# Performance work log

Measured on AMD Instinct MI355X. Metric: run time of the kernel, lower is better.

The kernel has to match this reference:

```python
import jax, jax.numpy as jnp
import numpy as np

B, S, E, H, VP, L, T = 256, 256, 1024, 1024, 8, 64, 16


def setup_inputs() -> dict:
    key = jax.random.key(0)
    ks = jax.random.split(key, 10)
    image = jax.random.normal(ks[0], (B, S, E), jnp.float32)
    view_position = jax.random.uniform(ks[1], (B, VP), jnp.float32)
    label = (jax.random.uniform(ks[2], (B, T + 1, L)) > 0.5).astype(jnp.float32)
    # lengths sorted descending (length_sorted_rnn decorator), max forced to T+1
    length = jnp.sort(jax.random.randint(ks[3], (B,), 2, T + 2))[::-1]
    length = length.at[0].set(T + 1)
    def lin(k, out_d, in_d):
        return jax.random.normal(k, (out_d, in_d), jnp.float32) * (1.0 / np.sqrt(in_d)).astype(np.float32)
    IN = E + VP + 1 + L  # 1097: lstm_sizes = [embedding, view_position, 1, label]
    FC_OUT = L + H + 1 + 1  # 1090: fc_sizes = [label, hidden, 1, 1]
    return {
        'image': image, 'view_position': view_position, 'label': label, 'length': length,
        'W_h': lin(ks[4], H, E), 'b_h': jnp.zeros((H,), jnp.float32),
        'W_m': lin(ks[5], H, E), 'b_m': jnp.zeros((H,), jnp.float32),
        'W_ih': lin(ks[6], 4 * H, IN), 'W_hh': lin(ks[7], 4 * H, H),
        'b_ih': jnp.zeros((4 * H,), jnp.float32), 'b_hh': jnp.zeros((4 * H,), jnp.float32),
        'W_fc': lin(ks[8], FC_OUT, H), 'b_fc': jnp.zeros((FC_OUT,), jnp.float32),
    }


def reference(image, view_position, label, length, W_h, b_h, W_m, b_m,
              W_ih, W_hh, b_ih, b_hh, W_fc, b_fc):
    # Dropout is identity (inference). image: (B,S,E)
    image_mean = image.mean(axis=1)                      # (B,E)
    h0 = jnp.tanh(image_mean @ W_h.T + b_h)              # (B,H)
    m0 = jnp.tanh(image_mean @ W_m.T + b_m)              # (B,H)
    n_steps = label.shape[1] - 1
    bsz = image_mean.shape[0]

    def step(carry, inp):
        h, m = carry
        lab_t, t = inp
        begin = jnp.where(t == 0, 1.0, 0.0) * jnp.ones((bsz, 1), image_mean.dtype)
        x = jnp.concatenate([image_mean, view_position, begin, lab_t], axis=1)  # (B, 1097)
        gates = x @ W_ih.T + b_ih + h @ W_hh.T + b_hh    # (B, 4H)
        i, f, g, o = jnp.split(gates, 4, axis=1)
        m2 = jax.nn.sigmoid(f) * m + jax.nn.sigmoid(i) * jnp.tanh(g)
        h2 = jax.nn.sigmoid(o) * jnp.tanh(m2)
        out = h2 @ W_fc.T + b_fc                         # (B, L+H+2)
        topic = jax.nn.relu(out[:, L:L + H])
        stop = jax.nn.sigmoid(out[:, L + H:L + H + 1])
        temp = jnp.exp(out[:, L + H + 1:])
        return (h2, m2), jnp.concatenate([topic, stop, temp], axis=1)

    labels_tm = jnp.swapaxes(label[:, :n_steps], 0, 1)   # (T,B,L) time-major
    _, outs = jax.lax.scan(step, (h0, m0), (labels_tm, jnp.arange(n_steps)))
    # pad_sequence semantics: entries with t >= length-1 are zero padding
    mask = (jnp.arange(n_steps)[:, None] < (length - 1)[None, :]).astype(outs.dtype)
    return outs * mask[:, :, None]                       # (T, B, H+2) = [topic|stop|temp]
```

## Files before the change

kernel.cpp:

```cpp
#include <hip/hip_runtime.h>
#include <stdint.h>

typedef unsigned short u16;
typedef __attribute__((ext_vector_type(8))) short v8s;
typedef __attribute__((ext_vector_type(4))) float v4f;

__device__ __forceinline__ u16 f2bf(float f) {
  uint32_t x = __float_as_uint(f);
  return (u16)((x + 0x7fffu + ((x >> 16) & 1u)) >> 16);
}
__device__ __forceinline__ float bf2f(u16 u) {
  return __uint_as_float(((uint32_t)u) << 16);
}
__device__ __forceinline__ float sigf(float x) { return 1.f / (1.f + __expf(-x)); }

__device__ __forceinline__ v4f mfma16(v8s a, v8s b, v4f c) {
  return __builtin_amdgcn_mfma_f32_16x16x32_bf16(a, b, c, 0, 0, 0);
}

__device__ __forceinline__ void gll16(const u16* src, u16* ldsdst) {
  __builtin_amdgcn_global_load_lds(
      reinterpret_cast<__attribute__((address_space(1))) uint32_t*>(
          reinterpret_cast<uintptr_t>(src)),
      reinterpret_cast<__attribute__((address_space(3))) uint32_t*>(
          reinterpret_cast<uintptr_t>(ldsdst)),
      16, 0, 0);
}

__device__ __forceinline__ size_t fpoff(int row, int k, int KT) {
  return ((size_t)(((row >> 4) * KT + (k >> 6)) * 2 + ((k >> 5) & 1)) * 64 +
          ((k >> 3) & 3) * 16 + (row & 15)) * 8 + (k & 7);
}

__device__ __forceinline__ void load8(const float* p, float* f) {
  float4 a = *(const float4*)p;
  float4 b = *(const float4*)(p + 4);
  f[0]=a.x; f[1]=a.y; f[2]=a.z; f[3]=a.w; f[4]=b.x; f[5]=b.y; f[6]=b.z; f[7]=b.w;
}
__device__ __forceinline__ void store8bf(u16* dst, const float* f) {
  u16 t[8];
#pragma unroll
  for (int i = 0; i < 8; ++i) t[i] = f2bf(f[i]);
  *(v8s*)dst = *(const v8s*)t;
}

__global__ __launch_bounds__(256) void k_zero(unsigned* __restrict__ ctr) {
  ctr[blockIdx.x * 256 + threadIdx.x] = 0u;
}

__global__ __launch_bounds__(256) void k_convert(
    const float* __restrict__ Wh, const float* __restrict__ Wm,
    const float* __restrict__ Wih, const float* __restrict__ Whh,
    const float* __restrict__ Wfc, const float* __restrict__ label,
    u16* __restrict__ wcomb, u16* __restrict__ whhb, u16* __restrict__ wfcb,
    u16* __restrict__ wlabb, u16* __restrict__ labb) {
  int64_t u = (int64_t)blockIdx.x * 256 + threadIdx.x;
  float f[8];
  if (u < 786432) {
    int lu = (int)u;
    int r15 = lu & 15, q = (lu >> 4) & 3, s = (lu >> 6) & 1, tile = lu >> 7;
    int tk = tile & 15, tr = tile >> 4;
    int row = tr * 16 + r15, k = tk * 64 + s * 32 + q * 8;
    if (row < 1024) load8(Wh + (size_t)row * 1024 + k, f);
    else if (row < 2048) load8(Wm + (size_t)(row - 1024) * 1024 + k, f);
    else {
      const float* p = Wih + (size_t)(row - 2048) * 1097 + k;
#pragma unroll
      for (int i = 0; i < 8; ++i) f[i] = p[i];
    }
    store8bf(wcomb + (size_t)lu * 8, f);
  } else if (u < 1310720) {
    int lu = (int)(u - 786432);
    int r15 = lu & 15, q = (lu >> 4) & 3, s = (lu >> 6) & 1, tile = lu >> 7;
    int tk = tile & 15, tr = tile >> 4;
    int row = tr * 16 + r15, k = tk * 64 + s * 32 + q * 8;
    load8(Whh + (size_t)row * 1024 + k, f);
    store8bf(whhb + (size_t)lu * 8, f);
  } else if (u < 1458176) {
    int lu = (int)(u - 1310720);
    int r15 = lu & 15, q = (lu >> 4) & 3, s = (lu >> 6) & 1, tile = lu >> 7;
    int tk = tile & 15, tr = tile >> 4;
    int row = tr * 16 + r15, k = tk * 64 + s * 32 + q * 8;
    if (row < 1090) load8(Wfc + (size_t)row * 1024 + k, f);
    else {
#pragma unroll
      for (int i = 0; i < 8; ++i) f[i] = 0.f;
    }
    store8bf(wfcb + (size_t)lu * 8, f);
  } else if (u < 1490944) {
    int lu = (int)(u - 1458176);
    int r15 = lu & 15, q = (lu >> 4) & 3, s = (lu >> 6) & 1, tile = lu >> 7;
    int row = tile * 16 + r15, k = s * 32 + q * 8;
    const float* p = Wih + (size_t)row * 1097 + 1033 + k;
#pragma unroll
    for (int i = 0; i < 8; ++i) f[i] = p[i];
    store8bf(wlabb + (size_t)lu * 8, f);
  } else {
    int lu = (int)(u - 1490944);
    int r15 = lu & 15, q = (lu >> 4) & 3, s = (lu >> 6) & 1, tile = lu >> 7;
    int row = tile * 16 + r15, k = s * 32 + q * 8;
    int t = row >> 8, b = row & 255;
    load8(label + ((size_t)b * 17 + t) * 64 + k, f);
    store8bf(labb + (size_t)lu * 8, f);
  }
}

__global__ __launch_bounds__(256) void k_mean1(const float* __restrict__ image,
                                               float4* __restrict__ pacc) {
  int bi = blockIdx.x;
  int b = bi >> 3, oct = bi & 7, tid = threadIdx.x;
  const float4* src = (const float4*)image + (size_t)b * 65536 + (size_t)oct * 32 * 256 + tid;
  float4 s = make_float4(0.f, 0.f, 0.f, 0.f);
#pragma unroll 8
  for (int ss = 0; ss < 32; ++ss) {
    float4 v = src[(size_t)ss * 256];
    s.x += v.x; s.y += v.y; s.z += v.z; s.w += v.w;
  }
  pacc[(size_t)bi * 256 + tid] = s;
}
__global__ __launch_bounds__(256) void k_mean2(const float4* __restrict__ pacc,
                                               u16* __restrict__ meanbf) {
  int b = blockIdx.x, tid = threadIdx.x;
  float4 s = make_float4(0.f, 0.f, 0.f, 0.f);
#pragma unroll
  for (int q = 0; q < 8; ++q) {
    float4 v = pacc[((size_t)b * 8 + q) * 256 + tid];
    s.x += v.x; s.y += v.y; s.z += v.z; s.w += v.w;
  }
  const float inv = 1.f / 256.f;
  int k = tid * 4;
  ushort4 o;
  o.x = f2bf(s.x * inv); o.y = f2bf(s.y * inv);
  o.z = f2bf(s.z * inv); o.w = f2bf(s.w * inv);
  *(ushort4*)&meanbf[fpoff(b, k, 16)] = o;
}

__global__ __launch_bounds__(256) void k_gemm_init(
    const u16* __restrict__ meanbf, const u16* __restrict__ wcomb,
    const float* __restrict__ bh, const float* __restrict__ bm,
    const float* __restrict__ bih, const float* __restrict__ bhh,
    const float* __restrict__ vp, const float* __restrict__ Wih,
    u16* __restrict__ hbuf, float* __restrict__ mbuf, float* __restrict__ basebuf) {
  __shared__ alignas(16) u16 lA[4 * 1024];
  __shared__ alignas(16) u16 lB[4 * 1024];
  const int tid = threadIdx.x, lane = tid & 63, wid = tid >> 6;
  const int bm0 = (blockIdx.x & 3) * 64;
  const int bn0 = (blockIdx.x >> 2) * 64;
  const int wr = wid >> 1, wc = wid & 1;
  v4f acc[2][2];
#pragma unroll
  for (int i = 0; i < 2; ++i)
#pragma unroll
    for (int j = 0; j < 2; ++j) acc[i][j] = (v4f){0.f, 0.f, 0.f, 0.f};

  for (int kt = 0; kt < 16; ++kt) {
    const u16* asrc = meanbf + ((size_t)((bm0 >> 4) + wid) * 16 + kt) * 1024 + lane * 8;
    gll16(asrc, lA + wid * 1024);
    gll16(asrc + 512, lA + wid * 1024 + 512);
    const u16* bsrc = wcomb + ((size_t)((bn0 >> 4) + wid) * 16 + kt) * 1024 + lane * 8;
    gll16(bsrc, lB + wid * 1024);
    gll16(bsrc + 512, lB + wid * 1024 + 512);
    __syncthreads();
#pragma unroll
    for (int s = 0; s < 2; ++s) {
      v8s a0 = *(const v8s*)&lA[(size_t)(wr * 2) * 1024 + s * 512 + lane * 8];
      v8s a1 = *(const v8s*)&lA[(size_t)(wr * 2 + 1) * 1024 + s * 512 + lane * 8];
      v8s b0 = *(const v8s*)&lB[(size_t)(wc * 2) * 1024 + s * 512 + lane * 8];
      v8s b1 = *(const v8s*)&lB[(size_t)(wc * 2 + 1) * 1024 + s * 512 + lane * 8];
      acc[0][0] = mfma16(a0, b0, acc[0][0]);
      acc[0][1] = mfma16(a0, b1, acc[0][1]);
      acc[1][0] = mfma16(a1, b0, acc[1][0]);
      acc[1][1] = mfma16(a1, b1, acc[1][1]);
    }
    __syncthreads();
  }
#pragma unroll
  for (int fm = 0; fm < 2; ++fm)
#pragma unroll
    for (int fn = 0; fn < 2; ++fn)
#pragma unroll
      for (int rg = 0; rg < 4; ++rg) {
        int row = bm0 + wr * 32 + fm * 16 + ((lane >> 4) << 2) + rg;
        int col = bn0 + wc * 32 + fn * 16 + (lane & 15);
        float v = acc[fm][fn][rg];
        if (col < 1024) {
          hbuf[fpoff(row, col, 16)] = f2bf(tanhf(v + bh[col]));
        } else if (col < 2048) {
          int nn = col - 1024;
          mbuf[(size_t)row * 1024 + nn] = tanhf(v + bm[nn]);
        } else {
          int j = col - 2048;
          float sv = v + bih[j] + bhh[j];
#pragma unroll
          for (int q = 0; q < 8; ++q)
            sv += vp[row * 8 + q] * Wih[(size_t)j * 1097 + 1024 + q];
          basebuf[(size_t)row * 4096 + j] = sv;
        }
      }
}

__global__ __launch_bounds__(256) void k_basefull(
    const u16* __restrict__ labb, const u16* __restrict__ wlabb,
    const float* __restrict__ basebuf, const float* __restrict__ Wih,
    u16* __restrict__ bfull) {
  __shared__ alignas(16) u16 lA[4 * 1024];
  __shared__ alignas(16) u16 lB[4 * 1024];
  const int tid = threadIdx.x, lane = tid & 63, wid = tid >> 6;
  const int bm0 = (blockIdx.x & 63) * 64;
  const int bn0 = (blockIdx.x >> 6) * 64;
  const int wr = wid >> 1, wc = wid & 1;
  v4f acc[2][2];
#pragma unroll
  for (int i = 0; i < 2; ++i)
#pragma unroll
    for (int j = 0; j < 2; ++j) acc[i][j] = (v4f){0.f, 0.f, 0.f, 0.f};

  const u16* asrc = labb + (size_t)((bm0 >> 4) + wid) * 1024 + lane * 8;
  gll16(asrc, lA + wid * 1024);
  gll16(asrc + 512, lA + wid * 1024 + 512);
  const u16* bsrc = wlabb + (size_t)((bn0 >> 4) + wid) * 1024 + lane * 8;
  gll16(bsrc, lB + wid * 1024);
  gll16(bsrc + 512, lB + wid * 1024 + 512);
  __syncthreads();
#pragma unroll
  for (int s = 0; s < 2; ++s) {
    v8s a0 = *(const v8s*)&lA[(size_t)(wr * 2) * 1024 + s * 512 + lane * 8];
    v8s a1 = *(const v8s*)&lA[(size_t)(wr * 2 + 1) * 1024 + s * 512 + lane * 8];
    v8s b0 = *(const v8s*)&lB[(size_t)(wc * 2) * 1024 + s * 512 + lane * 8];
    v8s b1 = *(const v8s*)&lB[(size_t)(wc * 2 + 1) * 1024 + s * 512 + lane * 8];
    acc[0][0] = mfma16(a0, b0, acc[0][0]);
    acc[0][1] = mfma16(a0, b1, acc[0][1]);
    acc[1][0] = mfma16(a1, b0, acc[1][0]);
    acc[1][1] = mfma16(a1, b1, acc[1][1]);
  }
#pragma unroll
  for (int fm = 0; fm < 2; ++fm)
#pragma unroll
    for (int fn = 0; fn < 2; ++fn)
#pragma unroll
      for (int rg = 0; rg < 4; ++rg) {
        int r = bm0 + wr * 32 + fm * 16 + ((lane >> 4) << 2) + rg;
        int j = bn0 + wc * 32 + fn * 16 + (lane & 15);
        int t = r >> 8, b = r & 255;
        float v = acc[fm][fn][rg] + basebuf[(size_t)b * 4096 + j];
        if (t == 0) v += Wih[(size_t)j * 1097 + 1032];
        bfull[(size_t)r * 4096 + j] = f2bf(v);
      }
}

__global__ __launch_bounds__(256, 1) void k_steps(
    const u16* __restrict__ whhb, const u16* __restrict__ bfull,
    const float* __restrict__ mbuf, u16* __restrict__ hbuf,
    unsigned* __restrict__ ctr) {
  __shared__ alignas(16) u16 lA[64 * 512];
  __shared__ alignas(16) float lact[4][32 * 33];
  const int tid = threadIdx.x, lane = tid & 63, wid = tid >> 6;
  const int blk = blockIdx.x;
  const int n0 = ((blk & 7) * 4 + (blk >> 6)) * 32;
  const int grp = (blk >> 3) & 7;
  const int b0 = grp * 32;
  const int atr = b0 >> 4;

  const int tr0 = wid * 64 + (n0 >> 4);
  v8s breg[16][2][2];
#pragma unroll
  for (int kt = 0; kt < 16; ++kt)
#pragma unroll
    for (int s = 0; s < 2; ++s)
#pragma unroll
      for (int j = 0; j < 2; ++j)
        breg[kt][s][j] =
            *(const v8s*)&whhb[((size_t)(tr0 + j) * 16 + kt) * 1024 + s * 512 + lane * 8];

  const int rowm = tid >> 3;
  const int nql = (tid & 7) * 4;
  const int b = b0 + rowm;
  const int n = n0 + nql;
  float4 mreg = *(const float4*)&mbuf[(size_t)b * 1024 + n];

  for (int t = 0; t < 16; ++t) {
    const u16* hsrc = hbuf + (size_t)t * 262144;
#pragma unroll
    for (int ii = 0; ii < 16; ++ii) {
      const int c = wid * 16 + ii;
      const int i = c >> 5, kt = (c >> 1) & 15, s = c & 1;
      gll16(hsrc + ((size_t)(atr + i) * 16 + kt) * 1024 + s * 512 + lane * 8,
            lA + c * 512);
    }
    const u16* bb = bfull + (size_t)t * 1048576 + (size_t)b * 4096 + n;
    ushort4 ui = *(const ushort4*)(bb);
    ushort4 uf = *(const ushort4*)(bb + 1024);
    ushort4 ug = *(const ushort4*)(bb + 2048);
    ushort4 uo = *(const ushort4*)(bb + 3072);
    __syncthreads();

    v4f acc[2][2];
#pragma unroll
    for (int i = 0; i < 2; ++i)
#pragma unroll
      for (int j = 0; j < 2; ++j) acc[i][j] = (v4f){0.f, 0.f, 0.f, 0.f};
#pragma unroll
    for (int kt = 0; kt < 16; ++kt)
#pragma unroll
      for (int s = 0; s < 2; ++s) {
        v8s a0 = *(const v8s*)&lA[(size_t)((0 * 16 + kt) * 2 + s) * 512 + lane * 8];
        v8s a1 = *(const v8s*)&lA[(size_t)((1 * 16 + kt) * 2 + s) * 512 + lane * 8];
        acc[0][0] = mfma16(a0, breg[kt][s][0], acc[0][0]);
        acc[0][1] = mfma16(a0, breg[kt][s][1], acc[0][1]);
        acc[1][0] = mfma16(a1, breg[kt][s][0], acc[1][0]);
        acc[1][1] = mfma16(a1, breg[kt][s][1], acc[1][1]);
      }

#pragma unroll
    for (int fm = 0; fm < 2; ++fm)
#pragma unroll
      for (int fn = 0; fn < 2; ++fn)
#pragma unroll
        for (int rg = 0; rg < 4; ++rg) {
          int rr = fm * 16 + ((lane >> 4) << 2) + rg;
          int cc = fn * 16 + (lane & 15);
          lact[wid][rr * 33 + cc] = acc[fm][fn][rg];
        }
    __syncthreads();

    float m2a[4];
    u16 h2a[4];
#pragma unroll
    for (int q = 0; q < 4; ++q) {
      float gi = lact[0][rowm * 33 + nql + q] + bf2f(((const u16*)&ui)[q]);
      float gf = lact[1][rowm * 33 + nql + q] + bf2f(((const u16*)&uf)[q]);
      float gg = lact[2][rowm * 33 + nql + q] + bf2f(((const u16*)&ug)[q]);
      float go = lact[3][rowm * 33 + nql + q] + bf2f(((const u16*)&uo)[q]);
      float mov = ((const float*)&mreg)[q];
      float m2 = sigf(gf) * mov + sigf(gi) * tanhf(gg);
      float h2 = sigf(go) * tanhf(m2);
      m2a[q] = m2;
      h2a[q] = f2bf(h2);
    }
    mreg = make_float4(m2a[0], m2a[1], m2a[2], m2a[3]);
    ushort4 ho;
    ho.x = h2a[0]; ho.y = h2a[1]; ho.z = h2a[2]; ho.w = h2a[3];
    unsigned long long hv;
    __builtin_memcpy(&hv, &ho, 8);
    __hip_atomic_store(
        reinterpret_cast<unsigned long long*>(
            &hbuf[(size_t)(t + 1) * 262144 + fpoff(b, n, 16)]),
        hv, __ATOMIC_RELAXED, __HIP_MEMORY_SCOPE_AGENT);

    if (t < 15) {
      __syncthreads();
      if (tid == 0) {
        unsigned* c = &ctr[(t * 8 + grp) * 32];
        __hip_atomic_fetch_add(c, 1u, __ATOMIC_RELAXED, __HIP_MEMORY_SCOPE_AGENT);
        for (int it = 0; it < (1 << 18); ++it) {
          unsigned v = __hip_atomic_load(c, __ATOMIC_RELAXED,
                                         __HIP_MEMORY_SCOPE_AGENT);
          if (v >= 32u) break;
          __builtin_amdgcn_s_sleep(2);
        }
      }
      __syncthreads();
    }
  }
}

__global__ __launch_bounds__(256) void k_fc(
    const u16* __restrict__ hall, const u16* __restrict__ wfcb,
    const float* __restrict__ bfc, const int* __restrict__ length,
    float* __restrict__ out) {
  __shared__ alignas(16) u16 lA[4 * 1024];
  __shared__ alignas(16) u16 lB[4 * 1024];
  const int tid = threadIdx.x, lane = tid & 63, wid = tid >> 6;
  const int bm0 = (int)(blockIdx.x % 64) * 64;
  const int bn0 = (int)(blockIdx.x / 64) * 64;
  const int wr = wid >> 1, wc = wid & 1;
  v4f acc[2][2];
#pragma unroll
  for (int i = 0; i < 2; ++i)
#pragma unroll
    for (int j = 0; j < 2; ++j) acc[i][j] = (v4f){0.f, 0.f, 0.f, 0.f};

  for (int kt = 0; kt < 16; ++kt) {
    const u16* asrc = hall + ((size_t)((bm0 >> 4) + wid) * 16 + kt) * 1024 + lane * 8;
    gll16(asrc, lA + wid * 1024);
    gll16(asrc + 512, lA + wid * 1024 + 512);
    const u16* bsrc = wfcb + ((size_t)((bn0 >> 4) + wid) * 16 + kt) * 1024 + lane * 8;
    gll16(bsrc, lB + wid * 1024);
    gll16(bsrc + 512, lB + wid * 1024 + 512);
    __syncthreads();
#pragma unroll
    for (int s = 0; s < 2; ++s) {
      v8s a0 = *(const v8s*)&lA[(size_t)(wr * 2) * 1024 + s * 512 + lane * 8];
      v8s a1 = *(const v8s*)&lA[(size_t)(wr * 2 + 1) * 1024 + s * 512 + lane * 8];
      v8s b0 = *(const v8s*)&lB[(size_t)(wc * 2) * 1024 + s * 512 + lane * 8];
      v8s b1 = *(const v8s*)&lB[(size_t)(wc * 2 + 1) * 1024 + s * 512 + lane * 8];
      acc[0][0] = mfma16(a0, b0, acc[0][0]);
      acc[0][1] = mfma16(a0, b1, acc[0][1]);
      acc[1][0] = mfma16(a1, b0, acc[1][0]);
      acc[1][1] = mfma16(a1, b1, acc[1][1]);
    }
    __syncthreads();
  }
#pragma unroll
  for (int fm = 0; fm < 2; ++fm)
#pragma unroll
    for (int fn = 0; fn < 2; ++fn)
#pragma unroll
      for (int rg = 0; rg < 4; ++rg) {
        int r = bm0 + wr * 32 + fm * 16 + ((lane >> 4) << 2) + rg;
        int j = bn0 + wc * 32 + fn * 16 + (lane & 15);
        if (j < 64 || j >= 1090) continue;
        int t = r >> 8, b = r & 255;
        float v = acc[fm][fn][rg] + bfc[j];
        int c;
        if (j < 1088) { c = j - 64; v = fmaxf(v, 0.f); }
        else if (j == 1088) { c = 1024; v = 1.f / (1.f + expf(-v)); }
        else { c = 1025; v = expf(v); }
        if (t >= length[b] - 1) v = 0.f;
        out[((size_t)t * 256 + b) * 1026 + c] = v;
      }
}

extern "C" void kernel_launch(void* const* d_in, const int* in_sizes, int n_in,
                              void* d_out, int out_size, void* d_ws, size_t ws_size,
                              hipStream_t stream) {
  (void)in_sizes; (void)n_in; (void)out_size; (void)ws_size;
  const float* image  = (const float*)d_in[0];
  const float* vp     = (const float*)d_in[1];
  const float* label  = (const float*)d_in[2];
  const int*   length = (const int*)d_in[3];
  const float* Wh  = (const float*)d_in[4];
  const float* bh  = (const float*)d_in[5];
  const float* Wm  = (const float*)d_in[6];
  const float* bm  = (const float*)d_in[7];
  const float* Wih = (const float*)d_in[8];
  const float* Whh = (const float*)d_in[9];
  const float* bih = (const float*)d_in[10];
  const float* bhh = (const float*)d_in[11];
  const float* Wfc = (const float*)d_in[12];
  const float* bfc = (const float*)d_in[13];
  float* out = (float*)d_out;
  char* ws = (char*)d_ws;

  size_t off = 0;
  u16* wcomb  = (u16*)(ws + off); off += (size_t)6144 * 1024 * 2;
  u16* whhb   = (u16*)(ws + off); off += (size_t)4096 * 1024 * 2;
  u16* wfcb   = (u16*)(ws + off); off += (size_t)1152 * 1024 * 2;
  u16* wlabb  = (u16*)(ws + off); off += (size_t)4096 * 64 * 2;
  u16* labb   = (u16*)(ws + off); off += (size_t)4096 * 64 * 2;
  u16* meanbf = (u16*)(ws + off); off += (size_t)256 * 1024 * 2;
  u16* hbuf   = (u16*)(ws + off); off += (size_t)17 * 256 * 1024 * 2;
  float* mbuf    = (float*)(ws + off); off += (size_t)256 * 1024 * 4;
  float* basebuf = (float*)(ws + off); off += (size_t)256 * 4096 * 4;
  u16* bfull  = (u16*)(ws + off); off += (size_t)16 * 256 * 4096 * 2;
  unsigned* ctr = (unsigned*)(ws + off); off += 4096 * 4;
  float4* pacc = (float4*)bfull;

  k_zero<<<16, 256, 0, stream>>>(ctr);
  k_convert<<<5952, 256, 0, stream>>>(Wh, Wm, Wih, Whh, Wfc, label,
                                      wcomb, whhb, wfcb, wlabb, labb);
  k_mean1<<<2048, 256, 0, stream>>>(image, pacc);
  k_mean2<<<256, 256, 0, stream>>>(pacc, meanbf);
  k_gemm_init<<<384, 256, 0, stream>>>(meanbf, wcomb, bh, bm, bih, bhh, vp, Wih,
                                       hbuf, mbuf, basebuf);
  k_basefull<<<4096, 256, 0, stream>>>(labb, wlabb, basebuf, Wih, bfull);
  k_steps<<<256, 256, 0, stream>>>(whhb, bfull, mbuf, hbuf, ctr);
  k_fc<<<1152, 256, 0, stream>>>(hbuf + (size_t)256 * 1024, wfcb, bfc, length, out);
}
```

Measured before the change: 232.3 us.

## Use per-block flags for step barrier and fuse image mean into convert kernel

The per-step inter-block barrier in the recurrent kernel changes from a shared atomic counter with spin-wait at the end of each step to per-block flag stores. Each wave then polls all 32 flags of its group with a ballot at the start of the next step, so one step's barrier wait can overlap the tail of the previous step and the fetch-add contention goes away. Separately, the image-mean partial-sum kernel is merged into the weight-conversion kernel as extra blocks, which saves a launch. The risk is memory ordering: flags are stored relaxed, and visibility of the hbuf writes relies on the earlier atomic stores plus the syncthreads.

```diff
diff --git a/kernel.cpp b/kernel.cpp
--- a/kernel.cpp
+++ b/kernel.cpp
@@ -48,13 +48,30 @@
   ctr[blockIdx.x * 256 + threadIdx.x] = 0u;
 }
 
-__global__ __launch_bounds__(256) void k_convert(
+__global__ __launch_bounds__(256) void k_convert_mean(
     const float* __restrict__ Wh, const float* __restrict__ Wm,
     const float* __restrict__ Wih, const float* __restrict__ Whh,
     const float* __restrict__ Wfc, const float* __restrict__ label,
+    const float* __restrict__ image,
     u16* __restrict__ wcomb, u16* __restrict__ whhb, u16* __restrict__ wfcb,
-    u16* __restrict__ wlabb, u16* __restrict__ labb) {
-  int64_t u = (int64_t)blockIdx.x * 256 + threadIdx.x;
+    u16* __restrict__ wlabb, u16* __restrict__ labb,
+    float4* __restrict__ pacc) {
+  const int bid = blockIdx.x, tid = threadIdx.x;
+  if (bid >= 5952) {
+    int bi = bid - 5952;
+    int b = bi >> 3, oct = bi & 7;
+    const float4* src =
+        (const float4*)image + (size_t)b * 65536 + (size_t)oct * 32 * 256 + tid;
+    float4 s = make_float4(0.f, 0.f, 0.f, 0.f);
+#pragma unroll 8
+    for (int ss = 0; ss < 32; ++ss) {
+      float4 v = src[(size_t)ss * 256];
+      s.x += v.x; s.y += v.y; s.z += v.z; s.w += v.w;
+    }
+    pacc[(size_t)bi * 256 + tid] = s;
+    return;
+  }
+  int64_t u = (int64_t)bid * 256 + tid;
   float f[8];
   if (u < 786432) {
     int lu = (int)u;
@@ -105,19 +122,6 @@
   }
 }
 
-__global__ __launch_bounds__(256) void k_mean1(const float* __restrict__ image,
-                                               float4* __restrict__ pacc) {
-  int bi = blockIdx.x;
-  int b = bi >> 3, oct = bi & 7, tid = threadIdx.x;
-  const float4* src = (const float4*)image + (size_t)b * 65536 + (size_t)oct * 32 * 256 + tid;
-  float4 s = make_float4(0.f, 0.f, 0.f, 0.f);
-#pragma unroll 8
-  for (int ss = 0; ss < 32; ++ss) {
-    float4 v = src[(size_t)ss * 256];
-    s.x += v.x; s.y += v.y; s.z += v.z; s.w += v.w;
-  }
-  pacc[(size_t)bi * 256 + tid] = s;
-}
 __global__ __launch_bounds__(256) void k_mean2(const float4* __restrict__ pacc,
                                                u16* __restrict__ meanbf) {
   int b = blockIdx.x, tid = threadIdx.x;
@@ -256,7 +260,8 @@
   __shared__ alignas(16) float lact[4][32 * 33];
   const int tid = threadIdx.x, lane = tid & 63, wid = tid >> 6;
   const int blk = blockIdx.x;
-  const int n0 = ((blk & 7) * 4 + (blk >> 6)) * 32;
+  const int n0idx = (blk & 7) * 4 + (blk >> 6);
+  const int n0 = n0idx * 32;
   const int grp = (blk >> 3) & 7;
   const int b0 = grp * 32;
   const int atr = b0 >> 4;
@@ -279,6 +284,15 @@
   float4 mreg = *(const float4*)&mbuf[(size_t)b * 1024 + n];
 
   for (int t = 0; t < 16; ++t) {
+    if (t > 0) {
+      const unsigned* f = &ctr[((t - 1) * 8 + grp) * 32];
+      for (int it = 0; it < (1 << 18); ++it) {
+        unsigned v = __hip_atomic_load(&f[lane & 31], __ATOMIC_RELAXED,
+                                       __HIP_MEMORY_SCOPE_AGENT);
+        if (__ballot(v == 0u) == 0ull) break;
+        __builtin_amdgcn_s_sleep(1);
+      }
+    }
     const u16* hsrc = hbuf + (size_t)t * 262144;
 #pragma unroll
     for (int ii = 0; ii < 16; ++ii) {
@@ -349,17 +363,9 @@
 
     if (t < 15) {
       __syncthreads();
-      if (tid == 0) {
-        unsigned* c = &ctr[(t * 8 + grp) * 32];
-        __hip_atomic_fetch_add(c, 1u, __ATOMIC_RELAXED, __HIP_MEMORY_SCOPE_AGENT);
-        for (int it = 0; it < (1 << 18); ++it) {
-          unsigned v = __hip_atomic_load(c, __ATOMIC_RELAXED,
-                                         __HIP_MEMORY_SCOPE_AGENT);
-          if (v >= 32u) break;
-          __builtin_amdgcn_s_sleep(2);
-        }
-      }
-      __syncthreads();
+      if (tid == 0)
+        __hip_atomic_store(&ctr[(t * 8 + grp) * 32 + n0idx], 1u,
+                           __ATOMIC_RELAXED, __HIP_MEMORY_SCOPE_AGENT);
     }
   }
 }
@@ -457,9 +463,8 @@
   float4* pacc = (float4*)bfull;
 
   k_zero<<<16, 256, 0, stream>>>(ctr);
-  k_convert<<<5952, 256, 0, stream>>>(Wh, Wm, Wih, Whh, Wfc, label,
-                                      wcomb, whhb, wfcb, wlabb, labb);
-  k_mean1<<<2048, 256, 0, stream>>>(image, pacc);
+  k_convert_mean<<<8000, 256, 0, stream>>>(Wh, Wm, Wih, Whh, Wfc, label, image,
+                                           wcomb, whhb, wfcb, wlabb, labb, pacc);
   k_mean2<<<256, 256, 0, stream>>>(pacc, meanbf);
   k_gemm_init<<<384, 256, 0, stream>>>(meanbf, wcomb, bh, bm, bih, bhh, vp, Wih,
                                        hbuf, mbuf, basebuf);
```

Result: no change. 232.2 us (-0.0%).
